# Optimization experiments

Hardware: AMD Instinct MI355X
Metric: run time of the kernel (lower is better)

Reference implementation:

```python
import jax, jax.numpy as jnp
import numpy as np

N = 262144
C_IN = 128
C_OUT = 128
K = 9


def setup_inputs() -> dict:
    key = jax.random.key(0)
    k1, k2, k3, k4 = jax.random.split(key, 4)
    features = jax.random.normal(k1, (N, C_IN), dtype=jnp.float32)
    neigh_idx = jax.random.randint(k2, (N, K), 0, N, dtype=jnp.int64)
    # nn.Linear(9*in_channels, out_channels): weight [out, 9*in], bias [out]
    fan_in = K * C_IN
    W = jax.random.normal(k3, (C_OUT, fan_in), dtype=jnp.float32) / np.sqrt(fan_in)
    b = jax.random.normal(k4, (C_OUT,), dtype=jnp.float32) * 0.01
    return {"features": features, "neigh_idx": neigh_idx, "W": W, "b": b}


def reference(features, neigh_idx, W, b):
    n = features.shape[0]
    # pad row of zeros at index n; redirect -1 neighbors to it
    feat_padded = jnp.concatenate([features, jnp.zeros((1, features.shape[1]), features.dtype)], axis=0)
    gather_idx = jnp.where(neigh_idx == -1, n, neigh_idx)
    col = feat_padded[gather_idx]              # [N, 9, C_in]
    col_flat = col.reshape(n, -1)              # [N, 9*C_in]
    return col_flat @ W.T + b                  # [N, C_out]
```

## Files before the change

### kernel.cpp

```cpp
#include <hip/hip_runtime.h>


#define NPTS    262144
#define CIN     128
#define COUT    128
#define KNBR    9
#define KDIM    (KNBR * CIN)
#define NKS     (KDIM / 16)
#define NFRAGS  (NKS * 4)
#define MT      128

typedef __bf16  bf16x8 __attribute__((ext_vector_type(8)));
typedef float   f32x4  __attribute__((ext_vector_type(4)));
typedef float   f32x16 __attribute__((ext_vector_type(16)));

__global__ __launch_bounds__(256) void pack_w_kernel(const float* __restrict__ W,
                                                     __bf16* __restrict__ Wp) {
    int t    = blockIdx.x * 256 + threadIdx.x;
    int lane = t & 63;
    int frag = t >> 6;
    if (frag >= NFRAGS) return;
    int nt = frag & 3;
    int ks = frag >> 2;
    int n  = nt * 32 + (lane & 31);
    int k0 = ks * 16 + (lane >> 5) * 8;
    const f32x4* src = (const f32x4*)(W + (size_t)n * KDIM + k0);
    f32x4 v0 = src[0], v1 = src[1];
    bf16x8 o;
#pragma unroll
    for (int i = 0; i < 4; ++i) { o[i] = (__bf16)v0[i]; o[i + 4] = (__bf16)v1[i]; }
    *(bf16x8*)(Wp + (size_t)frag * 512 + lane * 8) = o;
}

__global__ __launch_bounds__(256, 4) void qconv_kernel(
    const float*  __restrict__ feat,
    const int*    __restrict__ nidx,
    const __bf16* __restrict__ Wp,
    const float*  __restrict__ bias,
    float*        __restrict__ out)
{
    __shared__ __align__(16) __bf16 lds[32 * 512];

    const int tid  = threadIdx.x;
    const int lane = tid & 63;
    const int wave = tid >> 6;
    const int l31  = lane & 31;
    const int half = lane >> 5;
    const int row_base = blockIdx.x * MT + wave * 32;
    const int p = row_base + l31;

    f32x16 acc[4];
#pragma unroll
    for (int nt = 0; nt < 4; ++nt)
#pragma unroll
        for (int i = 0; i < 16; ++i) acc[nt][i] = 0.f;

    const int* nrow = nidx + (size_t)p * KNBR;

    for (int j = 0; j < KNBR; ++j) {
#pragma unroll
        for (int f8 = 0; f8 < 8; ++f8) {
            const int f = wave * 8 + f8;
            const __bf16* g = Wp + (size_t)(j * 32 + f) * 512 + lane * 8;
            __builtin_amdgcn_global_load_lds(
                (const __attribute__((address_space(1))) void*)g,
                (__attribute__((address_space(3))) void*)(lds + f * 512),
                16, 0, 0);
        }
        const int gi = nrow[j];
        const bool valid = gi >= 0;
        const float* arow = feat + (size_t)(valid ? gi : 0) * CIN;
        __syncthreads();

#pragma unroll
        for (int ks = 0; ks < 8; ++ks) {
            const int c0 = ks * 16 + half * 8;
            f32x4 a0 = {0.f, 0.f, 0.f, 0.f}, a1 = {0.f, 0.f, 0.f, 0.f};
            if (valid) {
                const f32x4* ap = (const f32x4*)(arow + c0);
                a0 = ap[0];
                a1 = ap[1];
            }
            bf16x8 afrag;
#pragma unroll
            for (int i = 0; i < 4; ++i) { afrag[i] = (__bf16)a0[i]; afrag[i + 4] = (__bf16)a1[i]; }
#pragma unroll
            for (int nt = 0; nt < 4; ++nt) {
                bf16x8 bfrag = *(const bf16x8*)(lds + (ks * 4 + nt) * 512 + lane * 8);
                acc[nt] = __builtin_amdgcn_mfma_f32_32x32x16_bf16(afrag, bfrag, acc[nt], 0, 0, 0);
            }
        }
        __syncthreads();
    }

#pragma unroll
    for (int nt = 0; nt < 4; ++nt) {
        const int col = nt * 32 + l31;
        const float bv = bias[col];
#pragma unroll
        for (int r = 0; r < 16; ++r) {
            const int row = (r & 3) + 8 * (r >> 2) + 4 * half;
            out[(size_t)(row_base + row) * COUT + col] = acc[nt][r] + bv;
        }
    }
}

extern "C" void kernel_launch(void* const* d_in, const int* in_sizes, int n_in,
                              void* d_out, int out_size, void* d_ws, size_t ws_size,
                              hipStream_t stream) {
    const float* feat = (const float*)d_in[0];
    const int*   nidx = (const int*)d_in[1];
    const float* W    = (const float*)d_in[2];
    const float* bias = (const float*)d_in[3];
    float*       out  = (float*)d_out;
    __bf16*      Wp   = (__bf16*)d_ws;

    pack_w_kernel<<<NFRAGS / 4, 256, 0, stream>>>(W, Wp);
    qconv_kernel<<<NPTS / MT, 256, 0, stream>>>(feat, nidx, Wp, bias, out);
}
```

Baseline: 412.8 us.

## Double-buffer weight tiles, prefetch gathered rows, and double rows per wave

Each wave now computes two 32-row tiles, so every weight fragment read from LDS feeds two MFMAs. Weight staging is double-buffered so the next neighbor's weights load while the current ones are consumed. Gathered feature rows are software-prefetched two k-steps ahead, across neighbor boundaries. Invalid neighbors now point at a zeroed workspace row instead of taking a branch. The cost is doubled accumulator registers (occupancy hint lowered to 2) and twice the LDS per block.

```diff
diff --git a/kernel.cpp b/kernel.cpp
--- a/kernel.cpp
+++ b/kernel.cpp
@@ -8,18 +8,23 @@
 #define KDIM    (KNBR * CIN)
 #define NKS     (KDIM / 16)
 #define NFRAGS  (NKS * 4)
-#define MT      128
+#define MT      256
+#define WP_ELEMS (NFRAGS * 512)
 
 typedef __bf16  bf16x8 __attribute__((ext_vector_type(8)));
 typedef float   f32x4  __attribute__((ext_vector_type(4)));
 typedef float   f32x16 __attribute__((ext_vector_type(16)));
 
 __global__ __launch_bounds__(256) void pack_w_kernel(const float* __restrict__ W,
-                                                     __bf16* __restrict__ Wp) {
+                                                     __bf16* __restrict__ Wp,
+                                                     float* __restrict__ zrow) {
+    if (blockIdx.x == NFRAGS / 4) {
+        if (threadIdx.x < CIN) zrow[threadIdx.x] = 0.f;
+        return;
+    }
     int t    = blockIdx.x * 256 + threadIdx.x;
     int lane = t & 63;
     int frag = t >> 6;
-    if (frag >= NFRAGS) return;
     int nt = frag & 3;
     int ks = frag >> 2;
     int n  = nt * 32 + (lane & 31);
@@ -32,64 +37,100 @@
     *(bf16x8*)(Wp + (size_t)frag * 512 + lane * 8) = o;
 }
 
-__global__ __launch_bounds__(256, 4) void qconv_kernel(
+struct ARegs { f32x4 r0a, r0b, r1a, r1b; };
+
+__global__ __launch_bounds__(256, 2) void qconv_kernel(
     const float*  __restrict__ feat,
     const int*    __restrict__ nidx,
     const __bf16* __restrict__ Wp,
+    const float*  __restrict__ zrow,
     const float*  __restrict__ bias,
     float*        __restrict__ out)
 {
-    __shared__ __align__(16) __bf16 lds[32 * 512];
+    __shared__ __align__(16) __bf16 lds[2][32 * 512];
 
     const int tid  = threadIdx.x;
     const int lane = tid & 63;
     const int wave = tid >> 6;
     const int l31  = lane & 31;
     const int half = lane >> 5;
-    const int row_base = blockIdx.x * MT + wave * 32;
-    const int p = row_base + l31;
+    const int rb   = blockIdx.x * MT;
+    const int p0   = rb + wave * 32 + l31;
+    const int p1   = p0 + 128;
 
-    f32x16 acc[4];
+    f32x16 acc[8];
 #pragma unroll
-    for (int nt = 0; nt < 4; ++nt)
+    for (int a = 0; a < 8; ++a)
 #pragma unroll
-        for (int i = 0; i < 16; ++i) acc[nt][i] = 0.f;
+        for (int i = 0; i < 16; ++i) acc[a][i] = 0.f;
 
-    const int* nrow = nidx + (size_t)p * KNBR;
+    const int* nrow0 = nidx + (size_t)p0 * KNBR;
+    const int* nrow1 = nidx + (size_t)p1 * KNBR;
 
-    for (int j = 0; j < KNBR; ++j) {
+    auto stage = [&](int j, int buf) {
 #pragma unroll
         for (int f8 = 0; f8 < 8; ++f8) {
             const int f = wave * 8 + f8;
             const __bf16* g = Wp + (size_t)(j * 32 + f) * 512 + lane * 8;
             __builtin_amdgcn_global_load_lds(
                 (const __attribute__((address_space(1))) void*)g,
-                (__attribute__((address_space(3))) void*)(lds + f * 512),
+                (__attribute__((address_space(3))) void*)(&lds[buf][f * 512 + lane * 8]),
                 16, 0, 0);
         }
-        const int gi = nrow[j];
-        const bool valid = gi >= 0;
-        const float* arow = feat + (size_t)(valid ? gi : 0) * CIN;
-        __syncthreads();
+    };
+    auto load_a = [&](const float* a0p, const float* a1p, int ks) -> ARegs {
+        const int c0 = ks * 16 + half * 8;
+        ARegs A;
+        A.r0a = *(const f32x4*)(a0p + c0);
+        A.r0b = *(const f32x4*)(a0p + c0 + 4);
+        A.r1a = *(const f32x4*)(a1p + c0);
+        A.r1b = *(const f32x4*)(a1p + c0 + 4);
+        return A;
+    };
+    auto cvt = [&](f32x4 a, f32x4 b) -> bf16x8 {
+        bf16x8 o;
+#pragma unroll
+        for (int i = 0; i < 4; ++i) { o[i] = (__bf16)a[i]; o[i + 4] = (__bf16)b[i]; }
+        return o;
+    };
+
+    int gi0 = nrow0[0], gi1 = nrow1[0];
+    const float* a0p = (gi0 >= 0) ? feat + (size_t)gi0 * CIN : zrow;
+    const float* a1p = (gi1 >= 0) ? feat + (size_t)gi1 * CIN : zrow;
+
+    stage(0, 0);
+    ARegs A0 = load_a(a0p, a1p, 0);
+    ARegs A1 = load_a(a0p, a1p, 1);
+    __syncthreads();
+
+    for (int j = 0; j < KNBR; ++j) {
+        const int buf = j & 1;
+        if (j + 1 < KNBR) stage(j + 1, buf ^ 1);
+        int ngi0 = (j + 1 < KNBR) ? nrow0[j + 1] : 0;
+        int ngi1 = (j + 1 < KNBR) ? nrow1[j + 1] : 0;
+        const float* na0p = (ngi0 >= 0) ? feat + (size_t)ngi0 * CIN : zrow;
+        const float* na1p = (ngi1 >= 0) ? feat + (size_t)ngi1 * CIN : zrow;
 
 #pragma unroll
         for (int ks = 0; ks < 8; ++ks) {
-            const int c0 = ks * 16 + half * 8;
-            f32x4 a0 = {0.f, 0.f, 0.f, 0.f}, a1 = {0.f, 0.f, 0.f, 0.f};
-            if (valid) {
-                const f32x4* ap = (const f32x4*)(arow + c0);
-                a0 = ap[0];
-                a1 = ap[1];
+            ARegs cur = (ks & 1) ? A1 : A0;
+            if (ks < 6) {
+                if (ks & 1) A1 = load_a(a0p, a1p, ks + 2);
+                else        A0 = load_a(a0p, a1p, ks + 2);
+            } else if (j + 1 < KNBR) {
+                if (ks & 1) A1 = load_a(na0p, na1p, ks - 6);
+                else        A0 = load_a(na0p, na1p, ks - 6);
             }
-            bf16x8 afrag;
-#pragma unroll
-            for (int i = 0; i < 4; ++i) { afrag[i] = (__bf16)a0[i]; afrag[i + 4] = (__bf16)a1[i]; }
+            bf16x8 af0 = cvt(cur.r0a, cur.r0b);
+            bf16x8 af1 = cvt(cur.r1a, cur.r1b);
 #pragma unroll
             for (int nt = 0; nt < 4; ++nt) {
-                bf16x8 bfrag = *(const bf16x8*)(lds + (ks * 4 + nt) * 512 + lane * 8);
-                acc[nt] = __builtin_amdgcn_mfma_f32_32x32x16_bf16(afrag, bfrag, acc[nt], 0, 0, 0);
+                bf16x8 bfrag = *(const bf16x8*)(&lds[buf][(ks * 4 + nt) * 512 + lane * 8]);
+                acc[nt]     = __builtin_amdgcn_mfma_f32_32x32x16_bf16(af0, bfrag, acc[nt], 0, 0, 0);
+                acc[4 + nt] = __builtin_amdgcn_mfma_f32_32x32x16_bf16(af1, bfrag, acc[4 + nt], 0, 0, 0);
             }
         }
+        a0p = na0p; a1p = na1p;
         __syncthreads();
     }
 
@@ -100,7 +141,8 @@
 #pragma unroll
         for (int r = 0; r < 16; ++r) {
             const int row = (r & 3) + 8 * (r >> 2) + 4 * half;
-            out[(size_t)(row_base + row) * COUT + col] = acc[nt][r] + bv;
+            out[(size_t)(rb + wave * 32 + row) * COUT + col]       = acc[nt][r] + bv;
+            out[(size_t)(rb + 128 + wave * 32 + row) * COUT + col] = acc[4 + nt][r] + bv;
         }
     }
 }
@@ -114,7 +156,8 @@
     const float* bias = (const float*)d_in[3];
     float*       out  = (float*)d_out;
     __bf16*      Wp   = (__bf16*)d_ws;
+    float*       zrow = (float*)((char*)d_ws + WP_ELEMS * 2);
 
-    pack_w_kernel<<<NFRAGS / 4, 256, 0, stream>>>(W, Wp);
-    qconv_kernel<<<NPTS / MT, 256, 0, stream>>>(feat, nidx, Wp, bias, out);
+    pack_w_kernel<<<NFRAGS / 4 + 1, 256, 0, stream>>>(W, Wp, zrow);
+    qconv_kernel<<<NPTS / MT, 256, 0, stream>>>(feat, nidx, Wp, zrow, bias, out);
 }
```

Measured after the change: 424.0 us. +2.7%, slower.

## Pre-convert features to bf16, double M tile, register-pipeline A/B loads without LDS

Applied to the files above, without the earlier changes.

Adds a pre-pass that converts the feature matrix to bf16 in workspace, so the gather reads half the bytes per neighbor row. The conv kernel now handles 256 rows per block (two 32-row tiles per wave, sharing B fragments). It replaces the LDS-staged weight loads and per-neighbor barriers with register-prefetched A and B fragments, loaded a few k-steps ahead. Invalid neighbors point to a zero row instead of being masked. This raises register pressure (launch bounds drop to 2 blocks) and adds an extra full pass over the features for the conversion.

```diff
diff --git a/kernel.cpp b/kernel.cpp
--- a/kernel.cpp
+++ b/kernel.cpp
@@ -8,18 +8,36 @@
 #define KDIM    (KNBR * CIN)
 #define NKS     (KDIM / 16)
 #define NFRAGS  (NKS * 4)
-#define MT      128
+#define MT      256
 
 typedef __bf16  bf16x8 __attribute__((ext_vector_type(8)));
 typedef float   f32x4  __attribute__((ext_vector_type(4)));
 typedef float   f32x16 __attribute__((ext_vector_type(16)));
 
+__global__ __launch_bounds__(256) void convert_feat_kernel(const float* __restrict__ f,
+                                                           __bf16* __restrict__ fb) {
+    size_t i = ((size_t)blockIdx.x * 256 + threadIdx.x) * 8;
+    f32x4 a = *(const f32x4*)(f + i);
+    f32x4 b = *(const f32x4*)(f + i + 4);
+    bf16x8 o;
+#pragma unroll
+    for (int k = 0; k < 4; ++k) { o[k] = (__bf16)a[k]; o[k + 4] = (__bf16)b[k]; }
+    *(bf16x8*)(fb + i) = o;
+}
+
 __global__ __launch_bounds__(256) void pack_w_kernel(const float* __restrict__ W,
-                                                     __bf16* __restrict__ Wp) {
+                                                     __bf16* __restrict__ Wp,
+                                                     float* __restrict__ zrow_f,
+                                                     __bf16* __restrict__ zrow_b) {
+    if (blockIdx.x == NFRAGS / 4) {
+        int t = threadIdx.x;
+        if (t < 128) zrow_f[t] = 0.f;
+        else         zrow_b[t - 128] = (__bf16)0.f;
+        return;
+    }
     int t    = blockIdx.x * 256 + threadIdx.x;
     int lane = t & 63;
     int frag = t >> 6;
-    if (frag >= NFRAGS) return;
     int nt = frag & 3;
     int ks = frag >> 2;
     int n  = nt * 32 + (lane & 31);
@@ -32,65 +50,91 @@
     *(bf16x8*)(Wp + (size_t)frag * 512 + lane * 8) = o;
 }
 
-__global__ __launch_bounds__(256, 4) void qconv_kernel(
-    const float*  __restrict__ feat,
+template <bool BF16A, typename AT>
+__global__ __launch_bounds__(256, 2) void qconv_kernel(
+    const AT*     __restrict__ featA,
     const int*    __restrict__ nidx,
     const __bf16* __restrict__ Wp,
+    const AT*     __restrict__ zrow,
     const float*  __restrict__ bias,
     float*        __restrict__ out)
 {
-    __shared__ __align__(16) __bf16 lds[32 * 512];
-
     const int tid  = threadIdx.x;
     const int lane = tid & 63;
     const int wave = tid >> 6;
     const int l31  = lane & 31;
     const int half = lane >> 5;
-    const int row_base = blockIdx.x * MT + wave * 32;
-    const int p = row_base + l31;
+    const int rb   = blockIdx.x * MT;
+    const int p0   = rb + wave * 32 + l31;
+    const int p1   = p0 + 128;
 
-    f32x16 acc[4];
+    const int* n0 = nidx + (size_t)p0 * KNBR;
+    const int* n1 = nidx + (size_t)p1 * KNBR;
+    const AT* pa0[KNBR];
+    const AT* pa1[KNBR];
 #pragma unroll
-    for (int nt = 0; nt < 4; ++nt)
+    for (int j = 0; j < KNBR; ++j) {
+        int g0 = n0[j], g1 = n1[j];
+        pa0[j] = (g0 >= 0) ? featA + (size_t)g0 * CIN : zrow;
+        pa1[j] = (g1 >= 0) ? featA + (size_t)g1 * CIN : zrow;
+    }
+
+    f32x16 acc[8];
 #pragma unroll
-        for (int i = 0; i < 16; ++i) acc[nt][i] = 0.f;
+    for (int a = 0; a < 8; ++a)
+#pragma unroll
+        for (int i = 0; i < 16; ++i) acc[a][i] = 0.f;
 
-    const int* nrow = nidx + (size_t)p * KNBR;
+    constexpr int AD = BF16A ? 4 : 2;
+    bf16x8 AbB[BF16A ? AD : 1][2];
+    f32x4  AbF[BF16A ? 1 : AD][2][2];
+    bf16x8 Bb[3][4];
 
-    for (int j = 0; j < KNBR; ++j) {
+    auto issueA = [&](int t) {
+        const int j = t >> 3, kk = t & 7;
+        const int off = kk * 16 + half * 8;
+        if constexpr (BF16A) {
+            AbB[t % AD][0] = *(const bf16x8*)((const __bf16*)pa0[j] + off);
+            AbB[t % AD][1] = *(const bf16x8*)((const __bf16*)pa1[j] + off);
+        } else {
+            AbF[t % AD][0][0] = *(const f32x4*)((const float*)pa0[j] + off);
+            AbF[t % AD][0][1] = *(const f32x4*)((const float*)pa0[j] + off + 4);
+            AbF[t % AD][1][0] = *(const f32x4*)((const float*)pa1[j] + off);
+            AbF[t % AD][1][1] = *(const f32x4*)((const float*)pa1[j] + off + 4);
+        }
+    };
+    auto getA = [&](int t, int tile) -> bf16x8 {
+        if constexpr (BF16A) {
+            return AbB[t % AD][tile];
+        } else {
+            f32x4 x = AbF[t % AD][tile][0], y = AbF[t % AD][tile][1];
+            bf16x8 o;
 #pragma unroll
-        for (int f8 = 0; f8 < 8; ++f8) {
-            const int f = wave * 8 + f8;
-            const __bf16* g = Wp + (size_t)(j * 32 + f) * 512 + lane * 8;
-            __builtin_amdgcn_global_load_lds(
-                (const __attribute__((address_space(1))) void*)g,
-                (__attribute__((address_space(3))) void*)(lds + f * 512),
-                16, 0, 0);
+            for (int k = 0; k < 4; ++k) { o[k] = (__bf16)x[k]; o[k + 4] = (__bf16)y[k]; }
+            return o;
         }
-        const int gi = nrow[j];
-        const bool valid = gi >= 0;
-        const float* arow = feat + (size_t)(valid ? gi : 0) * CIN;
-        __syncthreads();
+    };
+    auto issueB = [&](int t) {
+#pragma unroll
+        for (int nt = 0; nt < 4; ++nt)
+            Bb[t % 3][nt] = *(const bf16x8*)(Wp + (size_t)(t * 4 + nt) * 512 + lane * 8);
+    };
+
+    issueA(0); issueA(1);
+    if constexpr (BF16A) { issueA(2); issueA(3); }
+    issueB(0); issueB(1);
 
 #pragma unroll
-        for (int ks = 0; ks < 8; ++ks) {
-            const int c0 = ks * 16 + half * 8;
-            f32x4 a0 = {0.f, 0.f, 0.f, 0.f}, a1 = {0.f, 0.f, 0.f, 0.f};
-            if (valid) {
-                const f32x4* ap = (const f32x4*)(arow + c0);
-                a0 = ap[0];
-                a1 = ap[1];
-            }
-            bf16x8 afrag;
+    for (int t = 0; t < NKS; ++t) {
+        if (t + 2 < NKS) issueB(t + 2);
+        bf16x8 a0 = getA(t, 0);
+        bf16x8 a1 = getA(t, 1);
 #pragma unroll
-            for (int i = 0; i < 4; ++i) { afrag[i] = (__bf16)a0[i]; afrag[i + 4] = (__bf16)a1[i]; }
-#pragma unroll
-            for (int nt = 0; nt < 4; ++nt) {
-                bf16x8 bfrag = *(const bf16x8*)(lds + (ks * 4 + nt) * 512 + lane * 8);
-                acc[nt] = __builtin_amdgcn_mfma_f32_32x32x16_bf16(afrag, bfrag, acc[nt], 0, 0, 0);
-            }
+        for (int nt = 0; nt < 4; ++nt) {
+            acc[nt]     = __builtin_amdgcn_mfma_f32_32x32x16_bf16(a0, Bb[t % 3][nt], acc[nt], 0, 0, 0);
+            acc[4 + nt] = __builtin_amdgcn_mfma_f32_32x32x16_bf16(a1, Bb[t % 3][nt], acc[4 + nt], 0, 0, 0);
         }
-        __syncthreads();
+        if (t + AD < NKS) issueA(t + AD);
     }
 
 #pragma unroll
@@ -100,7 +144,8 @@
 #pragma unroll
         for (int r = 0; r < 16; ++r) {
             const int row = (r & 3) + 8 * (r >> 2) + 4 * half;
-            out[(size_t)(row_base + row) * COUT + col] = acc[nt][r] + bv;
+            out[(size_t)(rb + wave * 32 + row) * COUT + col]       = acc[nt][r] + bv;
+            out[(size_t)(rb + 128 + wave * 32 + row) * COUT + col] = acc[4 + nt][r] + bv;
         }
     }
 }
@@ -113,8 +158,23 @@
     const float* W    = (const float*)d_in[2];
     const float* bias = (const float*)d_in[3];
     float*       out  = (float*)d_out;
-    __bf16*      Wp   = (__bf16*)d_ws;
 
-    pack_w_kernel<<<NFRAGS / 4, 256, 0, stream>>>(W, Wp);
-    qconv_kernel<<<NPTS / MT, 256, 0, stream>>>(feat, nidx, Wp, bias, out);
+    const size_t FEATB_BYTES = (size_t)NPTS * CIN * 2;
+    const size_t WP_BYTES    = (size_t)NFRAGS * 512 * 2;
+
+    if (ws_size >= FEATB_BYTES + WP_BYTES + 1024) {
+        __bf16* featb  = (__bf16*)d_ws;
+        __bf16* Wp     = (__bf16*)((char*)d_ws + FEATB_BYTES);
+        float*  zrow_f = (float*)((char*)d_ws + FEATB_BYTES + WP_BYTES);
+        __bf16* zrow_b = (__bf16*)((char*)d_ws + FEATB_BYTES + WP_BYTES + 512);
+        convert_feat_kernel<<<NPTS * CIN / (256 * 8), 256, 0, stream>>>(feat, featb);
+        pack_w_kernel<<<NFRAGS / 4 + 1, 256, 0, stream>>>(W, Wp, zrow_f, zrow_b);
+        qconv_kernel<true, __bf16><<<NPTS / MT, 256, 0, stream>>>(featb, nidx, Wp, zrow_b, bias, out);
+    } else {
+        __bf16* Wp     = (__bf16*)d_ws;
+        float*  zrow_f = (float*)((char*)d_ws + WP_BYTES);
+        __bf16* zrow_b = (__bf16*)((char*)d_ws + WP_BYTES + 512);
+        pack_w_kernel<<<NFRAGS / 4 + 1, 256, 0, stream>>>(W, Wp, zrow_f, zrow_b);
+        qconv_kernel<false, float><<<NPTS / MT, 256, 0, stream>>>(feat, nidx, Wp, zrow_f, bias, out);
+    }
 }
```

Measured after the change: 372.3 us. -9.8%, faster.
